# Performance work log

Hardware: AMD Instinct MI355X
Metric: run time of the kernel (lower is better)

## Reference

```python
import jax, jax.numpy as jnp
import numpy as np

B, T, E, H, L = 32, 2048, 256, 256, 2


def setup_inputs() -> dict:
    key = jax.random.key(0)
    k = jax.random.split(key, 6)
    x = jax.random.normal(k[0], (B, T, E), jnp.float32)
    h0 = jax.random.normal(k[1], (L, B, H), jnp.float32)
    # weights scaled to avoid tanh saturation (mimics fan-in init)
    W0 = jax.random.normal(k[2], (E + H, H), jnp.float32) * 0.05
    b0 = jax.random.normal(k[3], (H,), jnp.float32) * 0.05
    W1 = jax.random.normal(k[4], (2 * H, H), jnp.float32) * 0.05
    b1 = jax.random.normal(k[5], (H,), jnp.float32) * 0.05
    return {"x": x, "h0": h0, "W0": W0, "b0": b0, "W1": W1, "b1": b1}


def reference(x, h0, W0, b0, W1, b1):
    # x: [B,T,E]; h0: [L,B,H] (torch permutes to [B,L,H])
    h_init = jnp.transpose(h0, (1, 0, 2))  # [B,L,H]
    Ws = (W0, W1)
    bs = (b0, b1)

    def step(h, x_t):  # h: [B,L,H], x_t: [B,E]
        inp = x_t
        new_h = []
        for l in range(L):  # small fixed stack of cells
            z = jnp.concatenate([inp, h[:, l, :]], axis=-1) @ Ws[l] + bs[l]
            ht = jnp.tanh(z)  # [B,H]
            inp = ht
            new_h.append(ht)
        return jnp.stack(new_h, axis=1), ht  # carry, per-step top-layer output

    x_tbe = jnp.transpose(x, (1, 0, 2))  # [T,B,E]
    h_final, outs = jax.lax.scan(step, h_init, x_tbe)
    hidden_states = jnp.transpose(outs, (1, 0, 2))  # [B,T,H]
    ht = h_final[:, -1:, :]  # final top-layer state, [B,1,H]
    return hidden_states, ht
```

## Files before the change

### kernel.cpp

```cpp
#include <hip/hip_runtime.h>


typedef _Float16 half2_t __attribute__((ext_vector_type(2)));

#define TT 2048
#define BB 32
#define XPB 8
#define CHUNK 64
#define NCHUNK (TT / CHUNK)

__device__ __forceinline__ unsigned packw(float lo, float hi) {
    half2_t r;
    r.x = (_Float16)lo;
    r.y = (_Float16)hi;
    return __builtin_bit_cast(unsigned, r);
}
#define H2(X) __builtin_bit_cast(half2_t, (X))

#define LDS_BARRIER() asm volatile("s_waitcnt lgkmcnt(0)\n\ts_barrier" ::: "memory")

__device__ __forceinline__ int rload(int* pf) {
    return __hip_atomic_load(pf, __ATOMIC_RELAXED, __HIP_MEMORY_SCOPE_AGENT);
}
__device__ __forceinline__ void astore(int* pf, int v) {
    __hip_atomic_store(pf, v, __ATOMIC_RELEASE, __HIP_MEMORY_SCOPE_AGENT);
}
#define ACQUIRE_FENCE() __builtin_amdgcn_fence(__ATOMIC_ACQUIRE, "agent")

#define KAW8(B)                                                             \
    "+v"(wp[(B)]), "+v"(wp[(B) + 1]), "+v"(wp[(B) + 2]), "+v"(wp[(B) + 3]), \
    "+v"(wp[(B) + 4]), "+v"(wp[(B) + 5]), "+v"(wp[(B) + 6]), "+v"(wp[(B) + 7])
#define KEEPALIVE()                                                  \
    asm volatile("" : KAW8(0), KAW8(8), KAW8(16), KAW8(24));         \
    asm volatile("" : KAW8(32), KAW8(40), KAW8(48), KAW8(56));       \
    asm volatile("" : KAW8(64), KAW8(72), KAW8(80), KAW8(88));       \
    asm volatile("" : KAW8(96), KAW8(104), KAW8(112), KAW8(120));

#define FDOT(H, W_, A) A = __builtin_amdgcn_fdot2(H2(H), H2(W_), A, false)
#define FD4(H, K)               \
    FDOT(H, wp[(K)], ac0);      \
    FDOT(H, wp[32 + (K)], ac1); \
    FDOT(H, wp[64 + (K)], ac2); \
    FDOT(H, wp[96 + (K)], ac3);

#define DOTS()                                                          \
    float ac0 = 0.f, ac1 = 0.f, ac2 = 0.f, ac3 = 0.f;                   \
    {                                                                   \
        const uint4* hp_ = hbq + 9 * p;                                 \
        uint4 q0 = hp_[0], q1 = hp_[1], q2 = hp_[2], q3 = hp_[3];       \
        uint4 q4 = hp_[4], q5 = hp_[5], q6 = hp_[6], q7 = hp_[7];       \
        FD4(q0.x, 0)  FD4(q0.y, 1)  FD4(q0.z, 2)  FD4(q0.w, 3)         \
        FD4(q1.x, 4)  FD4(q1.y, 5)  FD4(q1.z, 6)  FD4(q1.w, 7)         \
        FD4(q2.x, 8)  FD4(q2.y, 9)  FD4(q2.z, 10) FD4(q2.w, 11)        \
        FD4(q3.x, 12) FD4(q3.y, 13) FD4(q3.z, 14) FD4(q3.w, 15)        \
        FD4(q4.x, 16) FD4(q4.y, 17) FD4(q4.z, 18) FD4(q4.w, 19)        \
        FD4(q5.x, 20) FD4(q5.y, 21) FD4(q5.z, 22) FD4(q5.w, 23)        \
        FD4(q6.x, 24) FD4(q6.y, 25) FD4(q6.z, 26) FD4(q6.w, 27)        \
        FD4(q7.x, 28) FD4(q7.y, 29) FD4(q7.z, 30) FD4(q7.w, 31)        \
    }

#define BFLY(x)                                                              \
    asm("v_add_f32_dpp %0, %0, %0 quad_perm:[1,0,3,2] row_mask:0xf "         \
        "bank_mask:0xf"                                                      \
        : "+v"(x));                                                          \
    asm("v_add_f32_dpp %0, %0, %0 quad_perm:[2,3,0,1] row_mask:0xf "         \
        "bank_mask:0xf"                                                      \
        : "+v"(x));

#define LOAD_WP4(Wm, rowbase, p_, jg_)                                       \
    _Pragma("unroll")                                                        \
    for (int c = 0; c < 4; ++c) {                                            \
        _Pragma("unroll")                                                    \
        for (int k = 0; k < 32; ++k) {                                       \
            const int col_ = (jg_) + 64 * c;                                 \
            wp[c * 32 + k] =                                                 \
                packw((Wm)[(size_t)((rowbase) + 64 * (p_) + 2 * k) * 256 +   \
                           col_],                                            \
                      (Wm)[(size_t)((rowbase) + 64 * (p_) + 2 * k + 1) * 256 \
                           + col_]);                                         \
        }                                                                    \
    }

__device__ __forceinline__ int sidx_of(int i) {
    return 72 * (i >> 6) + (i & 63);
}

__device__ __forceinline__ void proj_rows(
    const float* __restrict__ src, float* __restrict__ dst,
    unsigned (&wp)[128], float bj, int nrows, uint4 (*hb)[36], int tid,
    int p, int jg, int col)
{
    _Float16* st0 = reinterpret_cast<_Float16*>(hb[0]);
    _Float16* st1 = reinterpret_cast<_Float16*>(hb[1]);
    const int si = sidx_of(tid);
    st0[si] = (_Float16)src[tid];
    __syncthreads();
    for (int r = 0; r < nrows; ++r) {
        KEEPALIVE()
        _Float16* stn = (r & 1) ? st0 : st1;
        if (r + 1 < nrows) stn[si] = (_Float16)src[(size_t)(r + 1) * 256 + tid];
        const uint4* hbq = hb[r & 1];
        DOTS()
        BFLY(ac0) BFLY(ac1) BFLY(ac2) BFLY(ac3)
        float z = (p == 0) ? ac0 : ((p == 1) ? ac1 : ((p == 2) ? ac2 : ac3));
        dst[(size_t)r * 256 + col] = z + bj;
        __syncthreads();
    }
}

template <int MODE>
__device__ __forceinline__ void scan_core(
    const float* __restrict__ W, const float* __restrict__ h_init,
    const float* __restrict__ xsrc, float* __restrict__ hdst, float* hfinal,
    int* pubflag, int* waitflags, uint4 (*hb)[36], int tid)
{
    const int p = tid & 3;
    const int jg = tid >> 2;
    const int col = jg + 64 * p;

    unsigned wp[128];
    LOAD_WP4(W, 256, p, jg)

    _Float16* hw0 = reinterpret_cast<_Float16*>(hb[0]);
    _Float16* hw1 = reinterpret_cast<_Float16*>(hb[1]);
    hw0[sidx_of(tid)] = (_Float16)h_init[tid];
    const int wsi = 72 * p + jg;

    float xpc[XPB], xpn[XPB], hs[XPB];

    auto step = [&](int t, float xp) -> float {
        KEEPALIVE()
        const uint4* hbq = hb[t & 1];
        DOTS()
        BFLY(ac0) BFLY(ac1) BFLY(ac2) BFLY(ac3)
        float z = (p == 0) ? ac0 : ((p == 1) ? ac1 : ((p == 2) ? ac2 : ac3));
        z += xp;
        const float e = __expf(2.0f * z);
        const float hn = 1.0f - 2.0f / (e + 1.0f);
        _Float16* dstw = ((t + 1) & 1) ? hw1 : hw0;
        dstw[wsi] = (_Float16)hn;
        LDS_BARRIER();
        return hn;
    };

    if (MODE != 2) {
#pragma unroll
        for (int u = 0; u < XPB; ++u) xpc[u] = xsrc[(size_t)u * 256 + col];
        __syncthreads();
        for (int t0 = 0; t0 < TT; t0 += XPB) {
            const bool more = (t0 + XPB) < TT;
            if (more) {
#pragma unroll
                for (int u = 0; u < XPB; ++u)
                    xpn[u] = xsrc[(size_t)(t0 + XPB + u) * 256 + col];
            }
#pragma unroll
            for (int u = 0; u < XPB; ++u) hs[u] = step(t0 + u, xpc[u]);
#pragma unroll
            for (int u = 0; u < XPB; ++u)
                hdst[(size_t)(t0 + u) * 256 + col] = hs[u];
            if (MODE == 1 && (((t0 + XPB) & (CHUNK - 1)) == 0)) {
                __syncthreads();
                if (tid == 0) astore(pubflag, t0 + XPB);
            }
            if (more) {
#pragma unroll
                for (int u = 0; u < XPB; ++u) xpc[u] = xpn[u];
            }
        }
        if (MODE == 0 && hfinal != nullptr) hfinal[col] = hs[XPB - 1];
    } else {
        __syncthreads();
        for (int chunk = 0; chunk < NCHUNK; ++chunk) {
            const int tbase = chunk * CHUNK;
            while (rload(&waitflags[chunk]) == 0) __builtin_amdgcn_s_sleep(1);
            ACQUIRE_FENCE();
#pragma unroll
            for (int u = 0; u < XPB; ++u)
                xpc[u] = xsrc[(size_t)(tbase + u) * 256 + col];
            for (int g = 0; g < CHUNK / XPB; ++g) {
                const int t0 = tbase + g * XPB;
                if (g + 1 < CHUNK / XPB) {
#pragma unroll
                    for (int u = 0; u < XPB; ++u)
                        xpn[u] = xsrc[(size_t)(t0 + XPB + u) * 256 + col];
                }
#pragma unroll
                for (int u = 0; u < XPB; ++u) hs[u] = step(t0 + u, xpc[u]);
#pragma unroll
                for (int u = 0; u < XPB; ++u)
                    hdst[(size_t)(t0 + u) * 256 + col] = hs[u];
                if (t0 + XPB == TT) hfinal[col] = hs[XPB - 1];
                if (g + 1 < CHUNK / XPB) {
#pragma unroll
                    for (int u = 0; u < XPB; ++u) xpc[u] = xpn[u];
                }
            }
        }
    }
}

__global__ __launch_bounds__(256, 1) void proj17_kernel(
    const float* in, const float* __restrict__ W, const float* __restrict__ bias,
    float* out, int rows_per_wg)
{
    __shared__ uint4 hb[2][36];
    const int tid = threadIdx.x;
    const int p = tid & 3;
    const int jg = tid >> 2;
    const int col = jg + 64 * p;
    unsigned wp[128];
    LOAD_WP4(W, 0, p, jg)
    const float bj = bias[col];
    const size_t r0 = (size_t)blockIdx.x * rows_per_wg;
    proj_rows(in + r0 * 256, out + r0 * 256, wp, bj, rows_per_wg, hb, tid, p,
              jg, col);
}

__global__ __launch_bounds__(256, 1) void scan17_kernel(
    const float* __restrict__ W, const float* __restrict__ h_init,
    float* __restrict__ io, float* __restrict__ hfinal)
{
    __shared__ uint4 hb[2][36];
    const int b = blockIdx.x;
    scan_core<0>(W, h_init + b * 256, io + (size_t)b * TT * 256,
                 io + (size_t)b * TT * 256,
                 hfinal ? hfinal + b * 256 : nullptr, nullptr, nullptr, hb,
                 threadIdx.x);
}

__global__ __launch_bounds__(256, 1) void mega17_kernel(
    const float* __restrict__ W0, const float* __restrict__ W1,
    const float* __restrict__ b1v, const float* __restrict__ h0init,
    float* xpA, float* out, int* flags)
{
    __shared__ uint4 hb[2][36];
    const int tid = threadIdx.x;
    const int bid = blockIdx.x;
    int* flagL0 = flags;
    int* chunkdone = flags + BB * 16;

    if (bid < BB) {
        const int b = bid;
        scan_core<1>(W0, h0init + b * 256, xpA + (size_t)b * TT * 256,
                     out + (size_t)b * TT * 256, nullptr, &flagL0[b * 16],
                     nullptr, hb, tid);
    } else if (bid >= 3 * BB) {
        const int b = bid - 3 * BB;
        scan_core<2>(W1, h0init + (size_t)(BB + b) * 256,
                     xpA + (size_t)b * TT * 256, out + (size_t)b * TT * 256,
                     out + (size_t)BB * TT * 256 + b * 256, nullptr,
                     &chunkdone[b * NCHUNK], hb, tid);
    } else {
        const int k = bid - BB;
        const int b = k >> 1;
        const int half = k & 1;
        const int p = tid & 3;
        const int jg = tid >> 2;
        const int col = jg + 64 * p;

        unsigned wp[128];
        LOAD_WP4(W1, 0, p, jg)
        const float bj = b1v[col];

        for (int chunk = half; chunk < NCHUNK; chunk += 2) {
            while (rload(&flagL0[b * 16]) < (chunk + 1) * CHUNK)
                __builtin_amdgcn_s_sleep(1);
            ACQUIRE_FENCE();
            const int tbase = chunk * CHUNK;
            const float* src = out + ((size_t)b * TT + tbase) * 256;
            float* dst = xpA + ((size_t)b * TT + tbase) * 256;
            proj_rows(src, dst, wp, bj, CHUNK, hb, tid, p, jg, col);
            __syncthreads();
            if (tid == 0) astore(&chunkdone[b * NCHUNK + chunk], 1);
        }
    }
}

extern "C" void kernel_launch(void* const* d_in, const int* in_sizes, int n_in,
                              void* d_out, int out_size, void* d_ws, size_t ws_size,
                              hipStream_t stream) {
    const float* x  = (const float*)d_in[0];
    const float* h0 = (const float*)d_in[1];
    const float* W0 = (const float*)d_in[2];
    const float* b0 = (const float*)d_in[3];
    const float* W1 = (const float*)d_in[4];
    const float* b1 = (const float*)d_in[5];
    float* out = (float*)d_out;

    const size_t XPA_FLOATS = (size_t)BB * TT * 256;
    const size_t FLAG_INTS = (size_t)BB * 16 + (size_t)BB * NCHUNK;
    const size_t NEEDED = XPA_FLOATS * 4 + FLAG_INTS * 4;

    if (ws_size >= NEEDED) {
        float* xpA = (float*)d_ws;
        int* flags = (int*)((char*)d_ws + XPA_FLOATS * 4);
        hipMemsetAsync(flags, 0, FLAG_INTS * 4, stream);
        proj17_kernel<<<256, 256, 0, stream>>>(x, W0, b0, xpA, 256);
        mega17_kernel<<<4 * BB, 256, 0, stream>>>(W0, W1, b1, h0, xpA, out, flags);
    } else {
        proj17_kernel<<<256, 256, 0, stream>>>(x, W0, b0, out, 256);
        scan17_kernel<<<BB, 256, 0, stream>>>(W0, h0, out, nullptr);
        proj17_kernel<<<256, 256, 0, stream>>>(out, W1, b1, out, 256);
        scan17_kernel<<<BB, 256, 0, stream>>>(W1, h0 + BB * 256, out, out + XPA_FLOATS);
    }
}
```

Baseline: 1.280 ms.

## Pack two batch scans per 512-thread workgroup and lighten projection barriers

```diff
diff --git a/kernel.cpp b/kernel.cpp
--- a/kernel.cpp
+++ b/kernel.cpp
@@ -85,6 +85,7 @@
     return 72 * (i >> 6) + (i & 63);
 }
 
+template <bool ALIAS>
 __device__ __forceinline__ void proj_rows(
     const float* __restrict__ src, float* __restrict__ dst,
     unsigned (&wp)[128], float bj, int nrows, uint4 (*hb)[36], int tid,
@@ -104,7 +105,8 @@
         BFLY(ac0) BFLY(ac1) BFLY(ac2) BFLY(ac3)
         float z = (p == 0) ? ac0 : ((p == 1) ? ac1 : ((p == 2) ? ac2 : ac3));
         dst[(size_t)r * 256 + col] = z + bj;
-        __syncthreads();
+        if (ALIAS) __syncthreads();
+        else LDS_BARRIER();
     }
 }
 
@@ -200,7 +202,8 @@
     }
 }
 
-__global__ __launch_bounds__(256, 1) void proj17_kernel(
+template <bool ALIAS>
+__global__ __launch_bounds__(256, 1) void proj18_kernel(
     const float* in, const float* __restrict__ W, const float* __restrict__ bias,
     float* out, int rows_per_wg)
 {
@@ -213,11 +216,11 @@
     LOAD_WP4(W, 0, p, jg)
     const float bj = bias[col];
     const size_t r0 = (size_t)blockIdx.x * rows_per_wg;
-    proj_rows(in + r0 * 256, out + r0 * 256, wp, bj, rows_per_wg, hb, tid, p,
-              jg, col);
-}
-
-__global__ __launch_bounds__(256, 1) void scan17_kernel(
+    proj_rows<ALIAS>(in + r0 * 256, out + r0 * 256, wp, bj, rows_per_wg, hb,
+                     tid, p, jg, col);
+}
+
+__global__ __launch_bounds__(256, 1) void scan18_kernel(
     const float* __restrict__ W, const float* __restrict__ h_init,
     float* __restrict__ io, float* __restrict__ hfinal)
 {
@@ -229,51 +232,53 @@
                  threadIdx.x);
 }
 
-__global__ __launch_bounds__(256, 1) void mega17_kernel(
+__global__ __launch_bounds__(512, 2) void mega18_kernel(
     const float* __restrict__ W0, const float* __restrict__ W1,
     const float* __restrict__ b1v, const float* __restrict__ h0init,
     float* xpA, float* out, int* flags)
 {
-    __shared__ uint4 hb[2][36];
+    __shared__ uint4 hb[2][2][36];
     const int tid = threadIdx.x;
+    const int half = tid >> 8;
+    const int ltid = tid & 255;
     const int bid = blockIdx.x;
     int* flagL0 = flags;
     int* chunkdone = flags + BB * 16;
 
-    if (bid < BB) {
-        const int b = bid;
+    if (bid < 16) {
+        const int b = bid * 2 + half;
         scan_core<1>(W0, h0init + b * 256, xpA + (size_t)b * TT * 256,
                      out + (size_t)b * TT * 256, nullptr, &flagL0[b * 16],
-                     nullptr, hb, tid);
-    } else if (bid >= 3 * BB) {
-        const int b = bid - 3 * BB;
-        scan_core<2>(W1, h0init + (size_t)(BB + b) * 256,
-                     xpA + (size_t)b * TT * 256, out + (size_t)b * TT * 256,
-                     out + (size_t)BB * TT * 256 + b * 256, nullptr,
-                     &chunkdone[b * NCHUNK], hb, tid);
-    } else {
-        const int k = bid - BB;
-        const int b = k >> 1;
-        const int half = k & 1;
-        const int p = tid & 3;
-        const int jg = tid >> 2;
+                     nullptr, hb[half], ltid);
+    } else if (bid < 48) {
+        const int b = bid - 16;
+        const int parity = half;
+        const int p = ltid & 3;
+        const int jg = ltid >> 2;
         const int col = jg + 64 * p;
 
         unsigned wp[128];
         LOAD_WP4(W1, 0, p, jg)
         const float bj = b1v[col];
 
-        for (int chunk = half; chunk < NCHUNK; chunk += 2) {
+        for (int chunk = parity; chunk < NCHUNK; chunk += 2) {
             while (rload(&flagL0[b * 16]) < (chunk + 1) * CHUNK)
                 __builtin_amdgcn_s_sleep(1);
             ACQUIRE_FENCE();
             const int tbase = chunk * CHUNK;
             const float* src = out + ((size_t)b * TT + tbase) * 256;
             float* dst = xpA + ((size_t)b * TT + tbase) * 256;
-            proj_rows(src, dst, wp, bj, CHUNK, hb, tid, p, jg, col);
+            proj_rows<false>(src, dst, wp, bj, CHUNK, hb[half], ltid, p, jg,
+                             col);
             __syncthreads();
-            if (tid == 0) astore(&chunkdone[b * NCHUNK + chunk], 1);
+            if (ltid == 0) astore(&chunkdone[b * NCHUNK + chunk], 1);
         }
+    } else {
+        const int b = (bid - 48) * 2 + half;
+        scan_core<2>(W1, h0init + (size_t)(BB + b) * 256,
+                     xpA + (size_t)b * TT * 256, out + (size_t)b * TT * 256,
+                     out + (size_t)BB * TT * 256 + b * 256, nullptr,
+                     &chunkdone[b * NCHUNK], hb[half], ltid);
     }
 }
 
@@ -296,12 +301,12 @@
         float* xpA = (float*)d_ws;
         int* flags = (int*)((char*)d_ws + XPA_FLOATS * 4);
         hipMemsetAsync(flags, 0, FLAG_INTS * 4, stream);
-        proj17_kernel<<<256, 256, 0, stream>>>(x, W0, b0, xpA, 256);
-        mega17_kernel<<<4 * BB, 256, 0, stream>>>(W0, W1, b1, h0, xpA, out, flags);
+        proj18_kernel<false><<<512, 256, 0, stream>>>(x, W0, b0, xpA, 128);
+        mega18_kernel<<<64, 512, 0, stream>>>(W0, W1, b1, h0, xpA, out, flags);
     } else {
-        proj17_kernel<<<256, 256, 0, stream>>>(x, W0, b0, out, 256);
-        scan17_kernel<<<BB, 256, 0, stream>>>(W0, h0, out, nullptr);
-        proj17_kernel<<<256, 256, 0, stream>>>(out, W1, b1, out, 256);
-        scan17_kernel<<<BB, 256, 0, stream>>>(W1, h0 + BB * 256, out, out + XPA_FLOATS);
-    }
-}
+        proj18_kernel<true><<<512, 256, 0, stream>>>(x, W0, b0, out, 128);
+        scan18_kernel<<<BB, 256, 0, stream>>>(W0, h0, out, nullptr);
+        proj18_kernel<true><<<512, 256, 0, stream>>>(out, W1, b1, out, 128);
+        scan18_kernel<<<BB, 256, 0, stream>>>(W1, h0 + BB * 256, out, out + XPA_FLOATS);
+    }
+}
```

New measurement: 1.951 ms. +52.4%, slower.

## Process two batch rows per scan workgroup and relax projection barriers

Applied to the files above, without the earlier changes.

```diff
diff --git a/kernel.cpp b/kernel.cpp
--- a/kernel.cpp
+++ b/kernel.cpp
@@ -36,27 +36,34 @@
     asm volatile("" : KAW8(64), KAW8(72), KAW8(80), KAW8(88));       \
     asm volatile("" : KAW8(96), KAW8(104), KAW8(112), KAW8(120));
 
-#define FDOT(H, W_, A) A = __builtin_amdgcn_fdot2(H2(H), H2(W_), A, false)
-#define FD4(H, K)               \
-    FDOT(H, wp[(K)], ac0);      \
-    FDOT(H, wp[32 + (K)], ac1); \
-    FDOT(H, wp[64 + (K)], ac2); \
-    FDOT(H, wp[96 + (K)], ac3);
-
-#define DOTS()                                                          \
-    float ac0 = 0.f, ac1 = 0.f, ac2 = 0.f, ac3 = 0.f;                   \
-    {                                                                   \
-        const uint4* hp_ = hbq + 9 * p;                                 \
-        uint4 q0 = hp_[0], q1 = hp_[1], q2 = hp_[2], q3 = hp_[3];       \
-        uint4 q4 = hp_[4], q5 = hp_[5], q6 = hp_[6], q7 = hp_[7];       \
-        FD4(q0.x, 0)  FD4(q0.y, 1)  FD4(q0.z, 2)  FD4(q0.w, 3)         \
-        FD4(q1.x, 4)  FD4(q1.y, 5)  FD4(q1.z, 6)  FD4(q1.w, 7)         \
-        FD4(q2.x, 8)  FD4(q2.y, 9)  FD4(q2.z, 10) FD4(q2.w, 11)        \
-        FD4(q3.x, 12) FD4(q3.y, 13) FD4(q3.z, 14) FD4(q3.w, 15)        \
-        FD4(q4.x, 16) FD4(q4.y, 17) FD4(q4.z, 18) FD4(q4.w, 19)        \
-        FD4(q5.x, 20) FD4(q5.y, 21) FD4(q5.z, 22) FD4(q5.w, 23)        \
-        FD4(q6.x, 24) FD4(q6.y, 25) FD4(q6.z, 26) FD4(q6.w, 27)        \
-        FD4(q7.x, 28) FD4(q7.y, 29) FD4(q7.z, 30) FD4(q7.w, 31)        \
+#define FDOTN(H, W_, A) A = __builtin_amdgcn_fdot2(H2(H), H2(W_), A, false)
+#define FD4N(H, K, a0, a1, a2, a3)   \
+    FDOTN(H, wp[(K)], a0);           \
+    FDOTN(H, wp[32 + (K)], a1);      \
+    FDOTN(H, wp[64 + (K)], a2);      \
+    FDOTN(H, wp[96 + (K)], a3);
+
+#define DOTSN(HBQ, a0, a1, a2, a3)                                       \
+    {                                                                    \
+        const uint4* hp_ = (HBQ) + 9 * p;                                \
+        uint4 q0 = hp_[0], q1 = hp_[1], q2 = hp_[2], q3 = hp_[3];        \
+        uint4 q4 = hp_[4], q5 = hp_[5], q6 = hp_[6], q7 = hp_[7];        \
+        FD4N(q0.x, 0, a0, a1, a2, a3)  FD4N(q0.y, 1, a0, a1, a2, a3)     \
+        FD4N(q0.z, 2, a0, a1, a2, a3)  FD4N(q0.w, 3, a0, a1, a2, a3)     \
+        FD4N(q1.x, 4, a0, a1, a2, a3)  FD4N(q1.y, 5, a0, a1, a2, a3)     \
+        FD4N(q1.z, 6, a0, a1, a2, a3)  FD4N(q1.w, 7, a0, a1, a2, a3)     \
+        FD4N(q2.x, 8, a0, a1, a2, a3)  FD4N(q2.y, 9, a0, a1, a2, a3)     \
+        FD4N(q2.z, 10, a0, a1, a2, a3) FD4N(q2.w, 11, a0, a1, a2, a3)    \
+        FD4N(q3.x, 12, a0, a1, a2, a3) FD4N(q3.y, 13, a0, a1, a2, a3)    \
+        FD4N(q3.z, 14, a0, a1, a2, a3) FD4N(q3.w, 15, a0, a1, a2, a3)    \
+        FD4N(q4.x, 16, a0, a1, a2, a3) FD4N(q4.y, 17, a0, a1, a2, a3)    \
+        FD4N(q4.z, 18, a0, a1, a2, a3) FD4N(q4.w, 19, a0, a1, a2, a3)    \
+        FD4N(q5.x, 20, a0, a1, a2, a3) FD4N(q5.y, 21, a0, a1, a2, a3)    \
+        FD4N(q5.z, 22, a0, a1, a2, a3) FD4N(q5.w, 23, a0, a1, a2, a3)    \
+        FD4N(q6.x, 24, a0, a1, a2, a3) FD4N(q6.y, 25, a0, a1, a2, a3)    \
+        FD4N(q6.z, 26, a0, a1, a2, a3) FD4N(q6.w, 27, a0, a1, a2, a3)    \
+        FD4N(q7.x, 28, a0, a1, a2, a3) FD4N(q7.y, 29, a0, a1, a2, a3)    \
+        FD4N(q7.z, 30, a0, a1, a2, a3) FD4N(q7.w, 31, a0, a1, a2, a3)    \
     }
 
 #define BFLY(x)                                                              \
@@ -85,6 +92,7 @@
     return 72 * (i >> 6) + (i & 63);
 }
 
+template <bool ALIAS>
 __device__ __forceinline__ void proj_rows(
     const float* __restrict__ src, float* __restrict__ dst,
     unsigned (&wp)[128], float bj, int nrows, uint4 (*hb)[36], int tid,
@@ -100,19 +108,24 @@
         _Float16* stn = (r & 1) ? st0 : st1;
         if (r + 1 < nrows) stn[si] = (_Float16)src[(size_t)(r + 1) * 256 + tid];
         const uint4* hbq = hb[r & 1];
-        DOTS()
+        float ac0 = 0.f, ac1 = 0.f, ac2 = 0.f, ac3 = 0.f;
+        DOTSN(hbq, ac0, ac1, ac2, ac3)
         BFLY(ac0) BFLY(ac1) BFLY(ac2) BFLY(ac3)
         float z = (p == 0) ? ac0 : ((p == 1) ? ac1 : ((p == 2) ? ac2 : ac3));
         dst[(size_t)r * 256 + col] = z + bj;
-        __syncthreads();
+        if (ALIAS) __syncthreads();
+        else LDS_BARRIER();
     }
 }
 
 template <int MODE>
-__device__ __forceinline__ void scan_core(
-    const float* __restrict__ W, const float* __restrict__ h_init,
-    const float* __restrict__ xsrc, float* __restrict__ hdst, float* hfinal,
-    int* pubflag, int* waitflags, uint4 (*hb)[36], int tid)
+__device__ __forceinline__ void scan_pair(
+    const float* __restrict__ W,
+    const float* __restrict__ hiA, const float* __restrict__ hiB,
+    const float* __restrict__ xsA, const float* __restrict__ xsB,
+    float* __restrict__ hdA, float* __restrict__ hdB,
+    float* hfA, float* hfB, int* pubA, int* pubB, int* wfA, int* wfB,
+    uint4 (*hbb)[2][36], int tid)
 {
     const int p = tid & 3;
     const int jg = tid >> 2;
@@ -121,86 +134,126 @@
     unsigned wp[128];
     LOAD_WP4(W, 256, p, jg)
 
-    _Float16* hw0 = reinterpret_cast<_Float16*>(hb[0]);
-    _Float16* hw1 = reinterpret_cast<_Float16*>(hb[1]);
-    hw0[sidx_of(tid)] = (_Float16)h_init[tid];
+    reinterpret_cast<_Float16*>(hbb[0][0])[sidx_of(tid)] = (_Float16)hiA[tid];
+    reinterpret_cast<_Float16*>(hbb[1][0])[sidx_of(tid)] = (_Float16)hiB[tid];
     const int wsi = 72 * p + jg;
 
-    float xpc[XPB], xpn[XPB], hs[XPB];
-
-    auto step = [&](int t, float xp) -> float {
+    float xcA[XPB], xnA[XPB], hsA[XPB];
+    float xcB[XPB], xnB[XPB], hsB[XPB];
+
+    auto step = [&](int t, float xpA, float xpB, float& oA, float& oB) {
         KEEPALIVE()
-        const uint4* hbq = hb[t & 1];
-        DOTS()
-        BFLY(ac0) BFLY(ac1) BFLY(ac2) BFLY(ac3)
-        float z = (p == 0) ? ac0 : ((p == 1) ? ac1 : ((p == 2) ? ac2 : ac3));
-        z += xp;
-        const float e = __expf(2.0f * z);
-        const float hn = 1.0f - 2.0f / (e + 1.0f);
-        _Float16* dstw = ((t + 1) & 1) ? hw1 : hw0;
-        dstw[wsi] = (_Float16)hn;
+        float aA0 = 0.f, aA1 = 0.f, aA2 = 0.f, aA3 = 0.f;
+        float aB0 = 0.f, aB1 = 0.f, aB2 = 0.f, aB3 = 0.f;
+        DOTSN(hbb[0][t & 1], aA0, aA1, aA2, aA3)
+        DOTSN(hbb[1][t & 1], aB0, aB1, aB2, aB3)
+        BFLY(aA0) BFLY(aA1) BFLY(aA2) BFLY(aA3)
+        BFLY(aB0) BFLY(aB1) BFLY(aB2) BFLY(aB3)
+        float zA = (p == 0) ? aA0 : ((p == 1) ? aA1 : ((p == 2) ? aA2 : aA3));
+        float zB = (p == 0) ? aB0 : ((p == 1) ? aB1 : ((p == 2) ? aB2 : aB3));
+        zA += xpA;
+        zB += xpB;
+        const float eA = __expf(2.0f * zA);
+        const float eB = __expf(2.0f * zB);
+        const float hA = 1.0f - 2.0f / (eA + 1.0f);
+        const float hB = 1.0f - 2.0f / (eB + 1.0f);
+        reinterpret_cast<_Float16*>(hbb[0][(t + 1) & 1])[wsi] = (_Float16)hA;
+        reinterpret_cast<_Float16*>(hbb[1][(t + 1) & 1])[wsi] = (_Float16)hB;
         LDS_BARRIER();
-        return hn;
+        oA = hA;
+        oB = hB;
     };
 
     if (MODE != 2) {
 #pragma unroll
-        for (int u = 0; u < XPB; ++u) xpc[u] = xsrc[(size_t)u * 256 + col];
+        for (int u = 0; u < XPB; ++u) {
+            xcA[u] = xsA[(size_t)u * 256 + col];
+            xcB[u] = xsB[(size_t)u * 256 + col];
+        }
         __syncthreads();
         for (int t0 = 0; t0 < TT; t0 += XPB) {
             const bool more = (t0 + XPB) < TT;
             if (more) {
 #pragma unroll
-                for (int u = 0; u < XPB; ++u)
-                    xpn[u] = xsrc[(size_t)(t0 + XPB + u) * 256 + col];
-            }
-#pragma unroll
-            for (int u = 0; u < XPB; ++u) hs[u] = step(t0 + u, xpc[u]);
+                for (int u = 0; u < XPB; ++u) {
+                    xnA[u] = xsA[(size_t)(t0 + XPB + u) * 256 + col];
+                    xnB[u] = xsB[(size_t)(t0 + XPB + u) * 256 + col];
+                }
+            }
 #pragma unroll
             for (int u = 0; u < XPB; ++u)
-                hdst[(size_t)(t0 + u) * 256 + col] = hs[u];
+                step(t0 + u, xcA[u], xcB[u], hsA[u], hsB[u]);
+#pragma unroll
+            for (int u = 0; u < XPB; ++u) {
+                hdA[(size_t)(t0 + u) * 256 + col] = hsA[u];
+                hdB[(size_t)(t0 + u) * 256 + col] = hsB[u];
+            }
             if (MODE == 1 && (((t0 + XPB) & (CHUNK - 1)) == 0)) {
                 __syncthreads();
-                if (tid == 0) astore(pubflag, t0 + XPB);
+                if (tid == 0) {
+                    astore(pubA, t0 + XPB);
+                    astore(pubB, t0 + XPB);
+                }
             }
             if (more) {
 #pragma unroll
-                for (int u = 0; u < XPB; ++u) xpc[u] = xpn[u];
-            }
-        }
-        if (MODE == 0 && hfinal != nullptr) hfinal[col] = hs[XPB - 1];
+                for (int u = 0; u < XPB; ++u) {
+                    xcA[u] = xnA[u];
+                    xcB[u] = xnB[u];
+                }
+            }
+        }
+        if (MODE == 0 && hfA != nullptr) {
+            hfA[col] = hsA[XPB - 1];
+            hfB[col] = hsB[XPB - 1];
+        }
     } else {
         __syncthreads();
         for (int chunk = 0; chunk < NCHUNK; ++chunk) {
             const int tbase = chunk * CHUNK;
-            while (rload(&waitflags[chunk]) == 0) __builtin_amdgcn_s_sleep(1);
+            while (rload(&wfA[chunk]) == 0 || rload(&wfB[chunk]) == 0)
+                __builtin_amdgcn_s_sleep(1);
             ACQUIRE_FENCE();
 #pragma unroll
-            for (int u = 0; u < XPB; ++u)
-                xpc[u] = xsrc[(size_t)(tbase + u) * 256 + col];
+            for (int u = 0; u < XPB; ++u) {
+                xcA[u] = xsA[(size_t)(tbase + u) * 256 + col];
+                xcB[u] = xsB[(size_t)(tbase + u) * 256 + col];
+            }
             for (int g = 0; g < CHUNK / XPB; ++g) {
                 const int t0 = tbase + g * XPB;
                 if (g + 1 < CHUNK / XPB) {
 #pragma unroll
-                    for (int u = 0; u < XPB; ++u)
-                        xpn[u] = xsrc[(size_t)(t0 + XPB + u) * 256 + col];
-                }
-#pragma unroll
-                for (int u = 0; u < XPB; ++u) hs[u] = step(t0 + u, xpc[u]);
+                    for (int u = 0; u < XPB; ++u) {
+                        xnA[u] = xsA[(size_t)(t0 + XPB + u) * 256 + col];
+                        xnB[u] = xsB[(size_t)(t0 + XPB + u) * 256 + col];
+                    }
+                }
 #pragma unroll
                 for (int u = 0; u < XPB; ++u)
-                    hdst[(size_t)(t0 + u) * 256 + col] = hs[u];
-                if (t0 + XPB == TT) hfinal[col] = hs[XPB - 1];
+                    step(t0 + u, xcA[u], xcB[u], hsA[u], hsB[u]);
+#pragma unroll
+                for (int u = 0; u < XPB; ++u) {
+                    hdA[(size_t)(t0 + u) * 256 + col] = hsA[u];
+                    hdB[(size_t)(t0 + u) * 256 + col] = hsB[u];
+                }
+                if (t0 + XPB == TT) {
+                    hfA[col] = hsA[XPB - 1];
+                    hfB[col] = hsB[XPB - 1];
+                }
                 if (g + 1 < CHUNK / XPB) {
 #pragma unroll
-                    for (int u = 0; u < XPB; ++u) xpc[u] = xpn[u];
-                }
-            }
-        }
-    }
-}
-
-__global__ __launch_bounds__(256, 1) void proj17_kernel(
+                    for (int u = 0; u < XPB; ++u) {
+                        xcA[u] = xnA[u];
+                        xcB[u] = xnB[u];
+                    }
+                }
+            }
+        }
+    }
+}
+
+template <bool ALIAS>
+__global__ __launch_bounds__(256, 1) void proj19_kernel(
     const float* in, const float* __restrict__ W, const float* __restrict__ bias,
     float* out, int rows_per_wg)
 {
@@ -213,46 +266,61 @@
     LOAD_WP4(W, 0, p, jg)
     const float bj = bias[col];
     const size_t r0 = (size_t)blockIdx.x * rows_per_wg;
-    proj_rows(in + r0 * 256, out + r0 * 256, wp, bj, rows_per_wg, hb, tid, p,
-              jg, col);
-}
-
-__global__ __launch_bounds__(256, 1) void scan17_kernel(
+    proj_rows<ALIAS>(in + r0 * 256, out + r0 * 256, wp, bj, rows_per_wg, hb,
+                     tid, p, jg, col);
+}
+
+__global__ __launch_bounds__(256, 1) void scan19_kernel(
     const float* __restrict__ W, const float* __restrict__ h_init,
     float* __restrict__ io, float* __restrict__ hfinal)
 {
-    __shared__ uint4 hb[2][36];
-    const int b = blockIdx.x;
-    scan_core<0>(W, h_init + b * 256, io + (size_t)b * TT * 256,
-                 io + (size_t)b * TT * 256,
-                 hfinal ? hfinal + b * 256 : nullptr, nullptr, nullptr, hb,
-                 threadIdx.x);
-}
-
-__global__ __launch_bounds__(256, 1) void mega17_kernel(
+    __shared__ uint4 hbb[2][2][36];
+    const int b0 = blockIdx.x * 2;
+    scan_pair<0>(W, h_init + b0 * 256, h_init + (b0 + 1) * 256,
+                 io + (size_t)b0 * TT * 256, io + (size_t)(b0 + 1) * TT * 256,
+                 io + (size_t)b0 * TT * 256, io + (size_t)(b0 + 1) * TT * 256,
+                 hfinal ? hfinal + b0 * 256 : nullptr,
+                 hfinal ? hfinal + (b0 + 1) * 256 : nullptr,
+                 nullptr, nullptr, nullptr, nullptr, hbb, threadIdx.x);
+}
+
+__global__ __launch_bounds__(256, 1) void mega19_kernel(
     const float* __restrict__ W0, const float* __restrict__ W1,
     const float* __restrict__ b1v, const float* __restrict__ h0init,
     float* xpA, float* out, int* flags)
 {
-    __shared__ uint4 hb[2][36];
     const int tid = threadIdx.x;
     const int bid = blockIdx.x;
     int* flagL0 = flags;
     int* chunkdone = flags + BB * 16;
 
-    if (bid < BB) {
-        const int b = bid;
-        scan_core<1>(W0, h0init + b * 256, xpA + (size_t)b * TT * 256,
-                     out + (size_t)b * TT * 256, nullptr, &flagL0[b * 16],
-                     nullptr, hb, tid);
-    } else if (bid >= 3 * BB) {
-        const int b = bid - 3 * BB;
-        scan_core<2>(W1, h0init + (size_t)(BB + b) * 256,
-                     xpA + (size_t)b * TT * 256, out + (size_t)b * TT * 256,
-                     out + (size_t)BB * TT * 256 + b * 256, nullptr,
-                     &chunkdone[b * NCHUNK], hb, tid);
+    if (bid < 16 || bid >= 80) {
+        __shared__ uint4 hbb[2][2][36];
+        if (bid < 16) {
+            const int b0 = bid * 2;
+            scan_pair<1>(W0, h0init + b0 * 256, h0init + (b0 + 1) * 256,
+                         xpA + (size_t)b0 * TT * 256,
+                         xpA + (size_t)(b0 + 1) * TT * 256,
+                         out + (size_t)b0 * TT * 256,
+                         out + (size_t)(b0 + 1) * TT * 256, nullptr, nullptr,
+                         &flagL0[b0 * 16], &flagL0[(b0 + 1) * 16], nullptr,
+                         nullptr, hbb, tid);
+        } else {
+            const int b0 = (bid - 80) * 2;
+            scan_pair<2>(W1, h0init + (size_t)(BB + b0) * 256,
+                         h0init + (size_t)(BB + b0 + 1) * 256,
+                         xpA + (size_t)b0 * TT * 256,
+                         xpA + (size_t)(b0 + 1) * TT * 256,
+                         out + (size_t)b0 * TT * 256,
+                         out + (size_t)(b0 + 1) * TT * 256,
+                         out + (size_t)BB * TT * 256 + b0 * 256,
+                         out + (size_t)BB * TT * 256 + (b0 + 1) * 256,
+                         nullptr, nullptr, &chunkdone[b0 * NCHUNK],
+                         &chunkdone[(b0 + 1) * NCHUNK], hbb, tid);
+        }
     } else {
-        const int k = bid - BB;
+        __shared__ uint4 hb[2][36];
+        const int k = bid - 16;
         const int b = k >> 1;
         const int half = k & 1;
         const int p = tid & 3;
@@ -270,7 +338,7 @@
             const int tbase = chunk * CHUNK;
             const float* src = out + ((size_t)b * TT + tbase) * 256;
             float* dst = xpA + ((size_t)b * TT + tbase) * 256;
-            proj_rows(src, dst, wp, bj, CHUNK, hb, tid, p, jg, col);
+            proj_rows<false>(src, dst, wp, bj, CHUNK, hb, tid, p, jg, col);
             __syncthreads();
             if (tid == 0) astore(&chunkdone[b * NCHUNK + chunk], 1);
         }
@@ -296,12 +364,13 @@
         float* xpA = (float*)d_ws;
         int* flags = (int*)((char*)d_ws + XPA_FLOATS * 4);
         hipMemsetAsync(flags, 0, FLAG_INTS * 4, stream);
-        proj17_kernel<<<256, 256, 0, stream>>>(x, W0, b0, xpA, 256);
-        mega17_kernel<<<4 * BB, 256, 0, stream>>>(W0, W1, b1, h0, xpA, out, flags);
+        proj19_kernel<false><<<512, 256, 0, stream>>>(x, W0, b0, xpA, 128);
+        mega19_kernel<<<96, 256, 0, stream>>>(W0, W1, b1, h0, xpA, out, flags);
     } else {
-        proj17_kernel<<<256, 256, 0, stream>>>(x, W0, b0, out, 256);
-        scan17_kernel<<<BB, 256, 0, stream>>>(W0, h0, out, nullptr);
-        proj17_kernel<<<256, 256, 0, stream>>>(out, W1, b1, out, 256);
-        scan17_kernel<<<BB, 256, 0, stream>>>(W1, h0 + BB * 256, out, out + XPA_FLOATS);
-    }
-}
+        proj19_kernel<true><<<512, 256, 0, stream>>>(x, W0, b0, out, 128);
+        scan19_kernel<<<16, 256, 0, stream>>>(W0, h0, out, nullptr);
+        proj19_kernel<true><<<512, 256, 0, stream>>>(out, W1, b1, out, 128);
+        scan19_kernel<<<16, 256, 0, stream>>>(W1, h0 + BB * 256, out,
+                                              out + XPA_FLOATS);
+    }
+}
```

Result: slower. 2.164 ms (+69.0%).

## Remap mega-kernel blocks across CUs and lighten projection barriers

Applied to the files above, without the earlier changes.

```diff
diff --git a/kernel.cpp b/kernel.cpp
--- a/kernel.cpp
+++ b/kernel.cpp
@@ -85,6 +85,7 @@
     return 72 * (i >> 6) + (i & 63);
 }
 
+template <bool ALIAS>
 __device__ __forceinline__ void proj_rows(
     const float* __restrict__ src, float* __restrict__ dst,
     unsigned (&wp)[128], float bj, int nrows, uint4 (*hb)[36], int tid,
@@ -104,7 +105,8 @@
         BFLY(ac0) BFLY(ac1) BFLY(ac2) BFLY(ac3)
         float z = (p == 0) ? ac0 : ((p == 1) ? ac1 : ((p == 2) ? ac2 : ac3));
         dst[(size_t)r * 256 + col] = z + bj;
-        __syncthreads();
+        if (ALIAS) __syncthreads();
+        else LDS_BARRIER();
     }
 }
 
@@ -200,7 +202,8 @@
     }
 }
 
-__global__ __launch_bounds__(256, 1) void proj17_kernel(
+template <bool ALIAS>
+__global__ __launch_bounds__(256, 1) void proj20_kernel(
     const float* in, const float* __restrict__ W, const float* __restrict__ bias,
     float* out, int rows_per_wg)
 {
@@ -213,11 +216,11 @@
     LOAD_WP4(W, 0, p, jg)
     const float bj = bias[col];
     const size_t r0 = (size_t)blockIdx.x * rows_per_wg;
-    proj_rows(in + r0 * 256, out + r0 * 256, wp, bj, rows_per_wg, hb, tid, p,
-              jg, col);
-}
-
-__global__ __launch_bounds__(256, 1) void scan17_kernel(
+    proj_rows<ALIAS>(in + r0 * 256, out + r0 * 256, wp, bj, rows_per_wg, hb,
+                     tid, p, jg, col);
+}
+
+__global__ __launch_bounds__(256, 1) void scan20_kernel(
     const float* __restrict__ W, const float* __restrict__ h_init,
     float* __restrict__ io, float* __restrict__ hfinal)
 {
@@ -229,32 +232,34 @@
                  threadIdx.x);
 }
 
-__global__ __launch_bounds__(256, 1) void mega17_kernel(
+__global__ __launch_bounds__(256, 2) void mega20_kernel(
     const float* __restrict__ W0, const float* __restrict__ W1,
     const float* __restrict__ b1v, const float* __restrict__ h0init,
     float* xpA, float* out, int* flags)
 {
-    __shared__ uint4 hb[2][36];
     const int tid = threadIdx.x;
     const int bid = blockIdx.x;
     int* flagL0 = flags;
     int* chunkdone = flags + BB * 16;
 
     if (bid < BB) {
+        __shared__ uint4 hb[2][36];
         const int b = bid;
         scan_core<1>(W0, h0init + b * 256, xpA + (size_t)b * TT * 256,
                      out + (size_t)b * TT * 256, nullptr, &flagL0[b * 16],
                      nullptr, hb, tid);
-    } else if (bid >= 3 * BB) {
-        const int b = bid - 3 * BB;
+    } else if (bid < 2 * BB) {
+        __shared__ uint4 hb[2][36];
+        const int b = bid - BB;
         scan_core<2>(W1, h0init + (size_t)(BB + b) * 256,
                      xpA + (size_t)b * TT * 256, out + (size_t)b * TT * 256,
                      out + (size_t)BB * TT * 256 + b * 256, nullptr,
                      &chunkdone[b * NCHUNK], hb, tid);
-    } else {
-        const int k = bid - BB;
-        const int b = k >> 1;
-        const int half = k & 1;
+    } else if (bid >= 256 && bid < 256 + 2 * BB) {
+        __shared__ uint4 hb[2][36];
+        const int k = bid - 256;
+        const int parity = (k < BB) ? 0 : 1;
+        const int b = (k < BB) ? k : (k - BB);
         const int p = tid & 3;
         const int jg = tid >> 2;
         const int col = jg + 64 * p;
@@ -263,14 +268,14 @@
         LOAD_WP4(W1, 0, p, jg)
         const float bj = b1v[col];
 
-        for (int chunk = half; chunk < NCHUNK; chunk += 2) {
+        for (int chunk = parity; chunk < NCHUNK; chunk += 2) {
             while (rload(&flagL0[b * 16]) < (chunk + 1) * CHUNK)
                 __builtin_amdgcn_s_sleep(1);
             ACQUIRE_FENCE();
             const int tbase = chunk * CHUNK;
             const float* src = out + ((size_t)b * TT + tbase) * 256;
             float* dst = xpA + ((size_t)b * TT + tbase) * 256;
-            proj_rows(src, dst, wp, bj, CHUNK, hb, tid, p, jg, col);
+            proj_rows<false>(src, dst, wp, bj, CHUNK, hb, tid, p, jg, col);
             __syncthreads();
             if (tid == 0) astore(&chunkdone[b * NCHUNK + chunk], 1);
         }
@@ -296,12 +301,12 @@
         float* xpA = (float*)d_ws;
         int* flags = (int*)((char*)d_ws + XPA_FLOATS * 4);
         hipMemsetAsync(flags, 0, FLAG_INTS * 4, stream);
-        proj17_kernel<<<256, 256, 0, stream>>>(x, W0, b0, xpA, 256);
-        mega17_kernel<<<4 * BB, 256, 0, stream>>>(W0, W1, b1, h0, xpA, out, flags);
+        proj20_kernel<false><<<512, 256, 0, stream>>>(x, W0, b0, xpA, 128);
+        mega20_kernel<<<512, 256, 0, stream>>>(W0, W1, b1, h0, xpA, out, flags);
     } else {
-        proj17_kernel<<<256, 256, 0, stream>>>(x, W0, b0, out, 256);
-        scan17_kernel<<<BB, 256, 0, stream>>>(W0, h0, out, nullptr);
-        proj17_kernel<<<256, 256, 0, stream>>>(out, W1, b1, out, 256);
-        scan17_kernel<<<BB, 256, 0, stream>>>(W1, h0 + BB * 256, out, out + XPA_FLOATS);
-    }
-}
+        proj20_kernel<true><<<512, 256, 0, stream>>>(x, W0, b0, out, 128);
+        scan20_kernel<<<BB, 256, 0, stream>>>(W0, h0, out, nullptr);
+        proj20_kernel<true><<<512, 256, 0, stream>>>(out, W1, b1, out, 128);
+        scan20_kernel<<<BB, 256, 0, stream>>>(W1, h0 + BB * 256, out, out + XPA_FLOATS);
+    }
+}
```

After: 1.417 ms. 10.7% more time.
